# Kernel optimization log

Measured on AMD Instinct MI355X. Metric: run time of the kernel, lower is better.

## Reference

```python
import jax, jax.numpy as jnp
import numpy as np

EMBED_DIM = 1024
NUM_HEADS = 16
HEAD_DIM = EMBED_DIM // NUM_HEADS
SCALE = HEAD_DIM ** -0.5


def setup_inputs() -> dict:
    key = jax.random.key(0)
    ks = jax.random.split(key, 5)
    B, N, C = 4, 2048, EMBED_DIM
    s = C ** -0.5
    return {
        "x": jax.random.normal(ks[0], (B, N, C), dtype=jnp.float32),
        "w_qkv": jax.random.normal(ks[1], (C, 3 * C), dtype=jnp.float32) * s,
        "b_qkv": jnp.zeros((3 * C,), dtype=jnp.float32),
        "w_proj": jax.random.normal(ks[2], (C, C), dtype=jnp.float32) * s,
        "b_proj": jnp.zeros((C,), dtype=jnp.float32),
    }


def reference(x, w_qkv, b_qkv, w_proj, b_proj):
    B, N, C = x.shape
    H, D = NUM_HEADS, HEAD_DIM
    qkv = x @ w_qkv + b_qkv                      # (B, N, 3C)
    qkv = qkv.reshape(B, N, 3, H, D)
    qkv = jnp.transpose(qkv, (2, 0, 3, 1, 4))    # (3, B, H, N, D)
    q, k, v = qkv[0], qkv[1], qkv[2]
    attn = jnp.einsum('bhnd,bhmd->bhnm', q, k) * SCALE
    attn = jax.nn.softmax(attn, axis=-1)
    out = jnp.einsum('bhnm,bhmd->bhnd', attn, v)  # (B, H, N, D)
    out = jnp.transpose(out, (0, 2, 1, 3)).reshape(B, N, C)
    return out @ w_proj + b_proj
```

## Files before the change

kernel.cpp:

```cpp
#include <hip/hip_runtime.h>

typedef __attribute__((ext_vector_type(8))) short short8v;
typedef __attribute__((ext_vector_type(4))) short short4v;
typedef __attribute__((ext_vector_type(4))) float float4v;
typedef __attribute__((ext_vector_type(4))) unsigned short ushort4v;
typedef __attribute__((ext_vector_type(8))) unsigned short ushort8v;

#define GLOBAL_AS __attribute__((address_space(1)))
#define LDS_AS __attribute__((address_space(3)))

__device__ __forceinline__ void async_cp16(const void* g, void* l) {
  __builtin_amdgcn_global_load_lds((const GLOBAL_AS void*)g, (LDS_AS void*)l, 16, 0, 0);
}

__device__ __forceinline__ unsigned short f2bf(float f) {
  unsigned u = __float_as_uint(f);
  u += 0x7fffu + ((u >> 16) & 1u);
  return (unsigned short)(u >> 16);
}

#if defined(__HIP_DEVICE_COMPILE__)
#if __has_builtin(__builtin_amdgcn_exp2f)
#define EXP2F(x) __builtin_amdgcn_exp2f(x)
#else
#define EXP2F(x) exp2f(x)
#endif
#else
#define EXP2F(x) exp2f(x)
#endif

#if defined(__HIP_DEVICE_COMPILE__) && __has_builtin(__builtin_amdgcn_cvt_pk_bf16_f32)
typedef __attribute__((ext_vector_type(2))) __bf16 bf16x2v;
__device__ __forceinline__ unsigned pk_bf16(float a, float b) {
  bf16x2v r = __builtin_amdgcn_cvt_pk_bf16_f32(a, b);
  return __builtin_bit_cast(unsigned, r);
}
#else
__device__ __forceinline__ unsigned pk_bf16(float a, float b) {
  return (unsigned)f2bf(a) | ((unsigned)f2bf(b) << 16);
}
#endif

#define MFMA_QK(a, b, c) __builtin_amdgcn_mfma_f32_16x16x32_bf16(a, b, c, 0, 0, 0)


__global__ __launch_bounds__(256) void cvt_f32_bf16(const float* __restrict__ src,
                                                    unsigned short* __restrict__ dst) {
  int i = blockIdx.x * 256 + threadIdx.x;
  float4 v = ((const float4*)src)[i];
  ushort4v o;
  o.x = f2bf(v.x); o.y = f2bf(v.y); o.z = f2bf(v.z); o.w = f2bf(v.w);
  ((ushort4v*)dst)[i] = o;
}

__global__ __launch_bounds__(256) void transpose_w(const float* __restrict__ src,
                                                   unsigned short* __restrict__ dst,
                                                   int K, int N) {
  __shared__ float tile[64][65];
  int k0 = blockIdx.x * 64, n0 = blockIdx.y * 64;
  int t = threadIdx.x;
  int tc = t & 15, tr = t >> 4;
#pragma unroll
  for (int p = 0; p < 4; p++) {
    int r = tr + p * 16;
    float4 v = *(const float4*)(src + (size_t)(k0 + r) * N + n0 + tc * 4);
    tile[r][tc * 4 + 0] = v.x; tile[r][tc * 4 + 1] = v.y;
    tile[r][tc * 4 + 2] = v.z; tile[r][tc * 4 + 3] = v.w;
  }
  __syncthreads();
#pragma unroll
  for (int p = 0; p < 4; p++) {
    int rn = tr + p * 16;
    ushort4v o;
    o.x = f2bf(tile[tc * 4 + 0][rn]);
    o.y = f2bf(tile[tc * 4 + 1][rn]);
    o.z = f2bf(tile[tc * 4 + 2][rn]);
    o.w = f2bf(tile[tc * 4 + 3][rn]);
    *(ushort4v*)(dst + (size_t)(n0 + rn) * K + k0 + tc * 4) = o;
  }
}

__device__ __forceinline__ void stage128x32(const unsigned short* __restrict__ src,
                                            unsigned short* dst, int r0, int k0, int tid) {
#pragma unroll
  for (int p = 0; p < 2; p++) {
    int idx = p * 256 + tid;
    int row = idx >> 2, s = idx & 3;
    int ch = s ^ ((row >> 1) & 3);
    async_cp16(src + (size_t)(r0 + row) * 1024 + k0 + ch * 8, dst + idx * 8);
  }
}


#define TT_STRIDE 136

__global__ __launch_bounds__(256) void gemm_qkv(const unsigned short* __restrict__ A,
                                                const unsigned short* __restrict__ BT,
                                                const float* __restrict__ bias,
                                                unsigned short* __restrict__ Qo,
                                                unsigned short* __restrict__ Ko,
                                                unsigned short* __restrict__ VTo) {
  __shared__ unsigned short smem[128 * TT_STRIDE];
  unsigned short* As = smem;
  unsigned short* Bs = smem + 4096;
  int tid = threadIdx.x;
  int lane = tid & 63, w = tid >> 6, g = lane >> 4, c = lane & 15;
  int m0 = blockIdx.x * 128, n0 = blockIdx.y * 128;
  int wm = (w & 1) * 64, wn = (w >> 1) * 64;
  float4v acc[4][4] = {};

  for (int k0 = 0; k0 < 1024; k0 += 32) {
    __syncthreads();
    stage128x32(A, As, m0, k0, tid);
    stage128x32(BT, Bs, n0, k0, tid);
    __syncthreads();
    short8v af[4], bf[4];
#pragma unroll
    for (int i = 0; i < 4; i++) {
      int r = wm + i * 16 + c;
      af[i] = *(const short8v*)(&As[r * 32 + (g ^ ((r >> 1) & 3)) * 8]);
    }
#pragma unroll
    for (int j = 0; j < 4; j++) {
      int r = wn + j * 16 + c;
      bf[j] = *(const short8v*)(&Bs[r * 32 + (g ^ ((r >> 1) & 3)) * 8]);
    }
#pragma unroll
    for (int i = 0; i < 4; i++)
#pragma unroll
      for (int j = 0; j < 4; j++)
        acc[i][j] = MFMA_QK(af[i], bf[j], acc[i][j]);
  }

  int which = n0 >> 10;
  if (which != 2) {
#pragma unroll
    for (int j = 0; j < 4; j++) {
      int ng = n0 + wn + j * 16 + c;
      float bv = bias[ng];
      int h = (ng & 1023) >> 6, d = ng & 63;
#pragma unroll
      for (int i = 0; i < 4; i++) {
#pragma unroll
        for (int r = 0; r < 4; r++) {
          int mg = m0 + wm + i * 16 + g * 4 + r;
          int b = mg >> 11, n = mg & 2047;
          float v = acc[i][j][r] + bv;
          if (which == 0)
            Qo[((size_t)(b * 16 + h) * 2048 + n) * 64 + d] = f2bf(v * 0.18033688011112042f);
          else
            Ko[((size_t)(b * 16 + h) * 2048 + n) * 64 + d] = f2bf(v);
        }
      }
    }
  } else {
    __syncthreads();
#pragma unroll
    for (int j = 0; j < 4; j++) {
      int nl = wn + j * 16 + c;
      float bv = bias[n0 + nl];
#pragma unroll
      for (int i = 0; i < 4; i++) {
        int ml = wm + i * 16 + g * 4;
        unsigned p0 = pk_bf16(acc[i][j][0] + bv, acc[i][j][1] + bv);
        unsigned p1 = pk_bf16(acc[i][j][2] + bv, acc[i][j][3] + bv);
        *(unsigned*)(smem + nl * TT_STRIDE + ml) = p0;
        *(unsigned*)(smem + nl * TT_STRIDE + ml + 2) = p1;
      }
    }
    __syncthreads();
    int rr = lane >> 4, tc = lane & 15;
    int P = tc & 3, g32 = tc >> 2;
    int b = m0 >> 11, mloc = m0 & 2047;
    int h0 = (n0 & 1023) >> 6;
#pragma unroll
    for (int s = 0; s < 8; s++) {
      int row = w * 32 + s * 4 + rr;
      int h = h0 + (row >> 6), d = row & 63;
      const unsigned short* bp = smem + row * TT_STRIDE + g32 * 32 + P * 4;
      union { unsigned long long q[2]; ushort8v v; } u;
      u.q[0] = *(const unsigned long long*)(bp);
      u.q[1] = *(const unsigned long long*)(bp + 16);
      size_t gaddr = ((size_t)(b * 16 + h) * 64 + d) * 2048 + mloc + g32 * 32 + P * 8;
      *(ushort8v*)(VTo + gaddr) = u.v;
    }
  }
}


#define NTOK 2048
#define BK 64

__global__ __launch_bounds__(256, 2) void attn_kernel(const unsigned short* __restrict__ Qg,
                                                      const unsigned short* __restrict__ Kg,
                                                      const unsigned short* __restrict__ VTg,
                                                      unsigned short* __restrict__ Og) {
  __shared__ unsigned short Ks[2][BK * 64];
  __shared__ unsigned short VTs[2][64 * BK];

  int tid = threadIdx.x;
  int lane = tid & 63, w = tid >> 6, g = lane >> 4, c = lane & 15;
  int id = blockIdx.x;
  int xcd = id & 7, within = id >> 3;
  int bh = xcd * 8 + (within >> 3);
  int q0 = (within & 7) * 256;

  const unsigned short* Qb = Qg + (size_t)bh * NTOK * 64;
  const unsigned short* Kb = Kg + (size_t)bh * NTOK * 64;
  const unsigned short* VTb = VTg + (size_t)bh * 64 * NTOK;

  short8v qf[4][2];
#pragma unroll
  for (int nt = 0; nt < 4; nt++)
#pragma unroll
    for (int kk = 0; kk < 2; kk++)
      qf[nt][kk] = *(const short8v*)(Qb + (size_t)(q0 + w * 64 + nt * 16 + c) * 64 +
                                     kk * 32 + g * 8);

  short8v ones8;
#pragma unroll
  for (int i = 0; i < 8; i++) ones8[i] = (short)0x3F80;

  float4v lacc[4] = {};
  float4v o[4][4] = {};

#pragma unroll
  for (int p = 0; p < 2; p++) {
    int idx = p * 256 + tid;
    int row = idx >> 3, ch = idx & 7;
    async_cp16(Kb + (size_t)row * 64 + ((ch ^ (row & 7)) * 8), &Ks[0][idx * 8]);
    async_cp16(VTb + (size_t)row * NTOK + ((ch ^ (row & 7)) * 8), &VTs[0][idx * 8]);
  }

  for (int it = 0; it < NTOK / BK; it++) {
    int pb = it & 1;
    __syncthreads();

    if (it + 1 < NTOK / BK) {
      int kt = (it + 1) * BK;
#pragma unroll
      for (int p = 0; p < 2; p++) {
        int idx = p * 256 + tid;
        int row = idx >> 3, ch = idx & 7;
        async_cp16(Kb + (size_t)(kt + row) * 64 + ((ch ^ (row & 7)) * 8),
                   &Ks[1 - pb][idx * 8]);
        async_cp16(VTb + (size_t)row * NTOK + kt + ((ch ^ (row & 7)) * 8),
                   &VTs[1 - pb][idx * 8]);
      }
    }

    const unsigned short* Kp = &Ks[pb][0];
    const unsigned short* Vp = &VTs[pb][0];

#pragma unroll
    for (int t = 0; t < 2; t++) {
      float4v st[2][4] = {};
      __builtin_amdgcn_s_setprio(1);
#pragma unroll
      for (int mth = 0; mth < 2; mth++) {
        int row = (t * 2 + mth) * 16 + c;
        short8v kf[2];
#pragma unroll
        for (int kk = 0; kk < 2; kk++) {
          int ch = (kk * 4 + g) ^ (row & 7);
          kf[kk] = *(const short8v*)(Kp + row * 64 + ch * 8);
        }
#pragma unroll
        for (int nt = 0; nt < 4; nt++)
#pragma unroll
          for (int kk = 0; kk < 2; kk++)
            st[mth][nt] = MFMA_QK(kf[kk], qf[nt][kk], st[mth][nt]);
      }
      __builtin_amdgcn_s_setprio(0);

      short8v pa8[4];
#pragma unroll
      for (int nt = 0; nt < 4; nt++) {
        float4v a = st[0][nt], b2 = st[1][nt];
        a.x = EXP2F(a.x); a.y = EXP2F(a.y); a.z = EXP2F(a.z); a.w = EXP2F(a.w);
        b2.x = EXP2F(b2.x); b2.y = EXP2F(b2.y); b2.z = EXP2F(b2.z); b2.w = EXP2F(b2.w);
        union { unsigned u[4]; short8v s; } cv;
        cv.u[0] = pk_bf16(a.x, a.y);
        cv.u[1] = pk_bf16(a.z, a.w);
        cv.u[2] = pk_bf16(b2.x, b2.y);
        cv.u[3] = pk_bf16(b2.z, b2.w);
        pa8[nt] = cv.s;
      }

      __builtin_amdgcn_s_setprio(1);
#pragma unroll
      for (int nt_o = 0; nt_o < 4; nt_o++) {
        int d = nt_o * 16 + c;
        int s = (t * 4 + g) ^ (d & 7);
        short8v vb8 = *(const short8v*)(Vp + d * BK + s * 8);
#pragma unroll
        for (int mt = 0; mt < 4; mt++)
          o[mt][nt_o] = MFMA_QK(pa8[mt], vb8, o[mt][nt_o]);
      }
#pragma unroll
      for (int mt = 0; mt < 4; mt++)
        lacc[mt] = MFMA_QK(pa8[mt], ones8, lacc[mt]);
      __builtin_amdgcn_s_setprio(0);
    }
  }

  int b = bh >> 4, h = bh & 15;
#pragma unroll
  for (int mt = 0; mt < 4; mt++) {
    float4v li;
#pragma unroll
    for (int r = 0; r < 4; r++) li[r] = 1.0f / lacc[mt][r];
#pragma unroll
    for (int nt_o = 0; nt_o < 4; nt_o++) {
      float4v v = o[mt][nt_o] * li;
      int col = h * 64 + nt_o * 16 + c;
      int rowbase = b * NTOK + q0 + w * 64 + mt * 16 + g * 4;
#pragma unroll
      for (int r = 0; r < 4; r++)
        Og[(size_t)(rowbase + r) * 1024 + col] = f2bf(v[r]);
    }
  }
}

__global__ __launch_bounds__(256) void gemm_proj(const unsigned short* __restrict__ A,
                                                 const unsigned short* __restrict__ BT,
                                                 const float* __restrict__ bias,
                                                 float* __restrict__ out) {
  __shared__ unsigned short As[128 * 32];
  __shared__ unsigned short Bs[128 * 32];
  int tid = threadIdx.x;
  int lane = tid & 63, w = tid >> 6, g = lane >> 4, c = lane & 15;
  int m0 = blockIdx.x * 128, n0 = blockIdx.y * 128;
  int wm = (w & 1) * 64, wn = (w >> 1) * 64;
  float4v acc[4][4] = {};

  for (int k0 = 0; k0 < 1024; k0 += 32) {
    __syncthreads();
    stage128x32(A, As, m0, k0, tid);
    stage128x32(BT, Bs, n0, k0, tid);
    __syncthreads();
    short8v af[4], bf[4];
#pragma unroll
    for (int i = 0; i < 4; i++) {
      int r = wm + i * 16 + c;
      af[i] = *(const short8v*)(&As[r * 32 + (g ^ ((r >> 1) & 3)) * 8]);
    }
#pragma unroll
    for (int j = 0; j < 4; j++) {
      int r = wn + j * 16 + c;
      bf[j] = *(const short8v*)(&Bs[r * 32 + (g ^ ((r >> 1) & 3)) * 8]);
    }
#pragma unroll
    for (int i = 0; i < 4; i++)
#pragma unroll
      for (int j = 0; j < 4; j++)
        acc[i][j] = MFMA_QK(af[i], bf[j], acc[i][j]);
  }

#pragma unroll
  for (int j = 0; j < 4; j++) {
    int ng = n0 + wn + j * 16 + c;
    float bv = bias[ng];
#pragma unroll
    for (int i = 0; i < 4; i++) {
#pragma unroll
      for (int r = 0; r < 4; r++) {
        int mg = m0 + wm + i * 16 + g * 4 + r;
        out[(size_t)mg * 1024 + ng] = acc[i][j][r] + bv;
      }
    }
  }
}


extern "C" void kernel_launch(void* const* d_in, const int* in_sizes, int n_in,
                              void* d_out, int out_size, void* d_ws, size_t ws_size,
                              hipStream_t stream) {
  (void)in_sizes; (void)n_in; (void)out_size; (void)ws_size;
  const float* x = (const float*)d_in[0];
  const float* w_qkv = (const float*)d_in[1];
  const float* b_qkv = (const float*)d_in[2];
  const float* w_proj = (const float*)d_in[3];
  const float* b_proj = (const float*)d_in[4];
  float* out = (float*)d_out;

  unsigned short* x_bf = (unsigned short*)d_ws;
  unsigned short* wqkvT = x_bf + (size_t)8192 * 1024;
  unsigned short* wprojT = wqkvT + (size_t)3072 * 1024;
  unsigned short* qws = wprojT + (size_t)1024 * 1024;
  unsigned short* kws = qws + (size_t)8388608;
  unsigned short* vtws = kws + (size_t)8388608;
  unsigned short* aws = vtws + (size_t)8388608;

  cvt_f32_bf16<<<8192, 256, 0, stream>>>(x, x_bf);
  transpose_w<<<dim3(16, 48), 256, 0, stream>>>(w_qkv, wqkvT, 1024, 3072);
  transpose_w<<<dim3(16, 16), 256, 0, stream>>>(w_proj, wprojT, 1024, 1024);
  gemm_qkv<<<dim3(64, 24), 256, 0, stream>>>(x_bf, wqkvT, b_qkv, qws, kws, vtws);
  attn_kernel<<<512, 256, 0, stream>>>(qws, kws, vtws, aws);
  gemm_proj<<<dim3(64, 8), 256, 0, stream>>>(aws, wprojT, b_proj, out);
}
```

Measured before the change: 276.9 us.

## Load K and V fragments directly from global memory instead of LDS staging

```diff
diff --git a/kernel.cpp b/kernel.cpp
--- a/kernel.cpp
+++ b/kernel.cpp
@@ -189,15 +189,11 @@
 
 
 #define NTOK 2048
-#define BK 64
 
 __global__ __launch_bounds__(256, 2) void attn_kernel(const unsigned short* __restrict__ Qg,
                                                       const unsigned short* __restrict__ Kg,
                                                       const unsigned short* __restrict__ VTg,
                                                       unsigned short* __restrict__ Og) {
-  __shared__ unsigned short Ks[2][BK * 64];
-  __shared__ unsigned short VTs[2][64 * BK];
-
   int tid = threadIdx.x;
   int lane = tid & 63, w = tid >> 6, g = lane >> 4, c = lane & 15;
   int id = blockIdx.x;
@@ -224,84 +220,58 @@
   float4v lacc[4] = {};
   float4v o[4][4] = {};
 
-#pragma unroll
-  for (int p = 0; p < 2; p++) {
-    int idx = p * 256 + tid;
-    int row = idx >> 3, ch = idx & 7;
-    async_cp16(Kb + (size_t)row * 64 + ((ch ^ (row & 7)) * 8), &Ks[0][idx * 8]);
-    async_cp16(VTb + (size_t)row * NTOK + ((ch ^ (row & 7)) * 8), &VTs[0][idx * 8]);
-  }
-
-  for (int it = 0; it < NTOK / BK; it++) {
-    int pb = it & 1;
-    __syncthreads();
-
-    if (it + 1 < NTOK / BK) {
-      int kt = (it + 1) * BK;
-#pragma unroll
-      for (int p = 0; p < 2; p++) {
-        int idx = p * 256 + tid;
-        int row = idx >> 3, ch = idx & 7;
-        async_cp16(Kb + (size_t)(kt + row) * 64 + ((ch ^ (row & 7)) * 8),
-                   &Ks[1 - pb][idx * 8]);
-        async_cp16(VTb + (size_t)row * NTOK + kt + ((ch ^ (row & 7)) * 8),
-                   &VTs[1 - pb][idx * 8]);
-      }
-    }
-
-    const unsigned short* Kp = &Ks[pb][0];
-    const unsigned short* Vp = &VTs[pb][0];
-
-#pragma unroll
-    for (int t = 0; t < 2; t++) {
-      float4v st[2][4] = {};
-      __builtin_amdgcn_s_setprio(1);
-#pragma unroll
-      for (int mth = 0; mth < 2; mth++) {
-        int row = (t * 2 + mth) * 16 + c;
-        short8v kf[2];
-#pragma unroll
-        for (int kk = 0; kk < 2; kk++) {
-          int ch = (kk * 4 + g) ^ (row & 7);
-          kf[kk] = *(const short8v*)(Kp + row * 64 + ch * 8);
-        }
-#pragma unroll
-        for (int nt = 0; nt < 4; nt++)
-#pragma unroll
-          for (int kk = 0; kk < 2; kk++)
-            st[mth][nt] = MFMA_QK(kf[kk], qf[nt][kk], st[mth][nt]);
-      }
-      __builtin_amdgcn_s_setprio(0);
-
-      short8v pa8[4];
-#pragma unroll
-      for (int nt = 0; nt < 4; nt++) {
-        float4v a = st[0][nt], b2 = st[1][nt];
-        a.x = EXP2F(a.x); a.y = EXP2F(a.y); a.z = EXP2F(a.z); a.w = EXP2F(a.w);
-        b2.x = EXP2F(b2.x); b2.y = EXP2F(b2.y); b2.z = EXP2F(b2.z); b2.w = EXP2F(b2.w);
-        union { unsigned u[4]; short8v s; } cv;
-        cv.u[0] = pk_bf16(a.x, a.y);
-        cv.u[1] = pk_bf16(a.z, a.w);
-        cv.u[2] = pk_bf16(b2.x, b2.y);
-        cv.u[3] = pk_bf16(b2.z, b2.w);
-        pa8[nt] = cv.s;
-      }
-
-      __builtin_amdgcn_s_setprio(1);
-#pragma unroll
-      for (int nt_o = 0; nt_o < 4; nt_o++) {
-        int d = nt_o * 16 + c;
-        int s = (t * 4 + g) ^ (d & 7);
-        short8v vb8 = *(const short8v*)(Vp + d * BK + s * 8);
-#pragma unroll
-        for (int mt = 0; mt < 4; mt++)
-          o[mt][nt_o] = MFMA_QK(pa8[mt], vb8, o[mt][nt_o]);
-      }
+  const unsigned short* kbase = Kb + c * 64 + g * 8;
+  const unsigned short* vbase = VTb + (size_t)c * 2048 + g * 8;
+
+#pragma unroll 2
+  for (int ch = 0; ch < 64; ch++) {
+    short8v kf[2][2];
+#pragma unroll
+    for (int mth = 0; mth < 2; mth++)
+#pragma unroll
+      for (int kk = 0; kk < 2; kk++)
+        kf[mth][kk] = *(const short8v*)(kbase + ch * 2048 + mth * 1024 + kk * 32);
+
+    short8v vb[4];
+#pragma unroll
+    for (int nt_o = 0; nt_o < 4; nt_o++)
+      vb[nt_o] = *(const short8v*)(vbase + (size_t)nt_o * 32768 + ch * 32);
+
+    float4v st[2][4] = {};
+    __builtin_amdgcn_s_setprio(1);
+#pragma unroll
+    for (int mth = 0; mth < 2; mth++)
+#pragma unroll
+      for (int nt = 0; nt < 4; nt++)
+#pragma unroll
+        for (int kk = 0; kk < 2; kk++)
+          st[mth][nt] = MFMA_QK(kf[mth][kk], qf[nt][kk], st[mth][nt]);
+    __builtin_amdgcn_s_setprio(0);
+
+    short8v pa8[4];
+#pragma unroll
+    for (int nt = 0; nt < 4; nt++) {
+      float4v a = st[0][nt], b2 = st[1][nt];
+      a.x = EXP2F(a.x); a.y = EXP2F(a.y); a.z = EXP2F(a.z); a.w = EXP2F(a.w);
+      b2.x = EXP2F(b2.x); b2.y = EXP2F(b2.y); b2.z = EXP2F(b2.z); b2.w = EXP2F(b2.w);
+      union { unsigned u[4]; short8v s; } cv;
+      cv.u[0] = pk_bf16(a.x, a.y);
+      cv.u[1] = pk_bf16(a.z, a.w);
+      cv.u[2] = pk_bf16(b2.x, b2.y);
+      cv.u[3] = pk_bf16(b2.z, b2.w);
+      pa8[nt] = cv.s;
+    }
+
+    __builtin_amdgcn_s_setprio(1);
+#pragma unroll
+    for (int nt_o = 0; nt_o < 4; nt_o++)
 #pragma unroll
       for (int mt = 0; mt < 4; mt++)
-        lacc[mt] = MFMA_QK(pa8[mt], ones8, lacc[mt]);
-      __builtin_amdgcn_s_setprio(0);
-    }
+        o[mt][nt_o] = MFMA_QK(pa8[mt], vb[nt_o], o[mt][nt_o]);
+#pragma unroll
+    for (int mt = 0; mt < 4; mt++)
+      lacc[mt] = MFMA_QK(pa8[mt], ones8, lacc[mt]);
+    __builtin_amdgcn_s_setprio(0);
   }
 
   int b = bh >> 4, h = bh & 15;
```

After: 314.2 us. +13.5%, slower.
